# Performance work log

Hardware: AMD Instinct MI355X
Metric: run time of the kernel (lower is better)

The kernel has to match this reference:

```python
import jax, jax.numpy as jnp
import numpy as np
from jax import lax

B = 2; H = 32; W = 32; C = 384
NH = 12; NG = 6; KK = 7; STRIDE = 1; ORF = 2.0
CG = C // NG; HC = C // NH; GH = NH // NG; HID = 4 * C
EPS = 1e-5


def layernorm(x, w, b):
    mu = jnp.mean(x, axis=-1, keepdims=True)
    var = jnp.mean((x - mu) ** 2, axis=-1, keepdims=True)
    return (x - mu) * lax.rsqrt(var + EPS) * w + b


def ref_points(Hk, Wk):
    # normalized reference grid in (-1,1), ordering (y, x) as in _get_ref_points
    ry = ((jnp.arange(Hk, dtype=jnp.float32) + 0.5) / Hk) * 2.0 - 1.0
    rx = ((jnp.arange(Wk, dtype=jnp.float32) + 0.5) / Wk) * 2.0 - 1.0
    return jnp.stack(jnp.meshgrid(ry, rx, indexing='ij'), axis=-1)  # (Hk, Wk, 2)


def grid_sample(img, grid):
    # torch F.grid_sample: bilinear, align_corners=True, padding_mode='zeros'
    # img: (N, Cc, Hi, Wi); grid: (N, ..., 2) with (x, y) in [-1, 1]
    N, Cc, Hi, Wi = img.shape
    out_shape = grid.shape[1:-1]
    g = grid.reshape(N, -1, 2)
    x = (g[..., 0] + 1.0) * 0.5 * (Wi - 1)
    y = (g[..., 1] + 1.0) * 0.5 * (Hi - 1)
    x0 = jnp.floor(x); y0 = jnp.floor(y)
    wx1 = x - x0; wy1 = y - y0
    flat = img.reshape(N, Cc, Hi * Wi)
    M = g.shape[1]
    def gather(ix, iy, wgt):
        valid = (ix >= 0) & (ix <= Wi - 1) & (iy >= 0) & (iy <= Hi - 1)
        idx = (jnp.clip(iy, 0, Hi - 1) * Wi + jnp.clip(ix, 0, Wi - 1)).astype(jnp.int32)
        vals = jnp.take_along_axis(flat, jnp.broadcast_to(idx[:, None, :], (N, Cc, M)), axis=2)
        return vals * (wgt * valid.astype(img.dtype))[:, None, :]
    out = (gather(x0, y0, (1 - wx1) * (1 - wy1))
           + gather(x0 + 1, y0, wx1 * (1 - wy1))
           + gather(x0, y0 + 1, (1 - wx1) * wy1)
           + gather(x0 + 1, y0 + 1, wx1 * wy1))
    return out.reshape((N, Cc) + out_shape)


def setup_inputs() -> dict:
    ks = jax.random.split(jax.random.key(0), 16)
    n = lambda k, s, sc=0.02: jax.random.normal(k, s, jnp.float32) * sc
    return dict(
        x=jax.random.normal(ks[0], (B, H * W, C), jnp.float32),
        norm1_w=jnp.ones((C,), jnp.float32), norm1_b=jnp.zeros((C,), jnp.float32),
        wq=n(ks[1], (C, C)), bq=jnp.zeros((C,), jnp.float32),
        wk=n(ks[2], (C, C)), bk=jnp.zeros((C,), jnp.float32),
        wv=n(ks[3], (C, C)), bv=jnp.zeros((C,), jnp.float32),
        wo=n(ks[4], (C, C)), bo=jnp.zeros((C,), jnp.float32),
        off_dw_w=n(ks[5], (CG, 1, KK, KK)), off_dw_b=jnp.zeros((CG,), jnp.float32),
        off_ln_w=jnp.ones((CG,), jnp.float32), off_ln_b=jnp.zeros((CG,), jnp.float32),
        off_pw_w=n(ks[6], (2, CG)),
        rpe_table=n(ks[7], (NH, 2 * H - 1, 2 * W - 1), 0.01),
        norm2_w=jnp.ones((C,), jnp.float32), norm2_b=jnp.zeros((C,), jnp.float32),
        fc1_w=n(ks[8], (HID, C)), fc1_b=jnp.zeros((HID,), jnp.float32),
        fc2_w=n(ks[9], (C, HID)), fc2_b=jnp.zeros((C,), jnp.float32),
    )


def reference(x, norm1_w, norm1_b, wq, bq, wk, bk, wv, bv, wo, bo,
              off_dw_w, off_dw_b, off_ln_w, off_ln_b, off_pw_w, rpe_table,
              norm2_w, norm2_b, fc1_w, fc1_b, fc2_w, fc2_b):
    Bx, L, Cx = x.shape
    shortcut = x
    xn = layernorm(x, norm1_w, norm1_b)
    xi = xn.reshape(Bx, H, W, Cx).transpose(0, 3, 1, 2)  # (B, C, H, W)

    # proj_q (1x1 conv)
    q = jnp.einsum('bchw,dc->bdhw', xi, wq) + bq[None, :, None, None]

    # offset network on per-group channels
    q_off = q.reshape(Bx * NG, CG, H, W)
    o = lax.conv_general_dilated(q_off, off_dw_w, (STRIDE, STRIDE),
                                 [(KK // 2, KK // 2), (KK // 2, KK // 2)],
                                 dimension_numbers=('NCHW', 'OIHW', 'NCHW'),
                                 feature_group_count=CG) + off_dw_b[None, :, None, None]
    o = layernorm(o.transpose(0, 2, 3, 1), off_ln_w, off_ln_b)  # (Bg, Hk, Wk, CG)
    o = jax.nn.gelu(o, approximate=False)
    offset = jnp.einsum('bhwc,pc->bphw', o, off_pw_w)  # (Bg, 2, Hk, Wk)
    Hk, Wk = offset.shape[2], offset.shape[3]
    ns = Hk * Wk
    orange = jnp.array([1.0 / Hk, 1.0 / Wk], jnp.float32).reshape(1, 2, 1, 1)
    offset = jnp.tanh(offset) * orange * ORF
    offset = offset.transpose(0, 2, 3, 1)  # (Bg, Hk, Wk, 2) (y, x)
    pos = offset + ref_points(Hk, Wk)[None]  # offset_range_factor >= 0 branch

    # deformable sampling of the (normed) feature map
    xs = grid_sample(xi.reshape(Bx * NG, CG, H, W), pos[..., ::-1])  # (Bg, CG, Hk, Wk)
    xs = xs.reshape(Bx, Cx, 1, ns)

    k = (jnp.einsum('bcxn,dc->bdxn', xs, wk) + bk[None, :, None, None]).reshape(Bx * NH, HC, ns)
    v = (jnp.einsum('bcxn,dc->bdxn', xs, wv) + bv[None, :, None, None]).reshape(Bx * NH, HC, ns)
    q_ = q.reshape(Bx * NH, HC, H * W)

    attn = jnp.einsum('bcm,bcn->bmn', q_, k) * (HC ** -0.5)  # (B*NH, HW, ns)

    # continuous relative position bias via grid_sample on rpe_table
    rpe = jnp.broadcast_to(rpe_table[None], (Bx, NH, 2 * H - 1, 2 * W - 1)).reshape(
        Bx * NG, GH, 2 * H - 1, 2 * W - 1)
    qg = ref_points(H, W).reshape(H * W, 2)[None]  # (1, HW, 2)
    disp = (qg[:, :, None, :] - pos.reshape(Bx * NG, ns, 2)[:, None, :, :]) * 0.5  # (Bg, HW, ns, 2)
    bias = grid_sample(rpe, disp[..., ::-1])  # (Bg, GH, HW, ns)
    attn = attn + bias.reshape(Bx * NH, H * W, ns)

    attn = jax.nn.softmax(attn, axis=2)
    out = jnp.einsum('bmn,bcn->bcm', attn, v).reshape(Bx, Cx, H, W)
    y = jnp.einsum('bchw,dc->bdhw', out, wo) + bo[None, :, None, None]
    y = y.transpose(0, 2, 3, 1).reshape(Bx, L, Cx)

    x2 = shortcut + y
    h = layernorm(x2, norm2_w, norm2_b)
    h = jax.nn.gelu(h @ fc1_w.T + fc1_b, approximate=False) @ fc2_w.T + fc2_b
    return x2 + h
```

## Files before the change

### kernel.cpp

```cpp
#include <hip/hip_runtime.h>
#include <math.h>

#define Bc 2
#define Hh 32
#define Ww 32
#define Cc 384
#define NHc 12
#define NGc 6
#define CGc 64
#define HCc 32
#define GHc 2
#define HIDc 1536
#define Lc 1024
#define NSc 1024
#define BGc 12

typedef float f32x4 __attribute__((ext_vector_type(4)));
typedef short bf16x8 __attribute__((ext_vector_type(8)));

__device__ __forceinline__ float gelu_f(float v) {
    return 0.5f * v * (1.f + erff(v * 0.70710678118654752440f));
}

__device__ __forceinline__ unsigned short f2bf(float f) {
    unsigned u = __float_as_uint(f);
    u = (u + 0x7FFF + ((u >> 16) & 1)) >> 16;
    return (unsigned short)u;
}

__device__ __forceinline__ float bf2f(unsigned short u) {
    return __uint_as_float((unsigned)u << 16);
}

__global__ __launch_bounds__(128) void ln_kernel(
    const float* __restrict__ x, const float* __restrict__ w,
    const float* __restrict__ b, unsigned short* __restrict__ out)
{
    __shared__ float l1[2], l2[2];
    int row = blockIdx.x;
    int t = threadIdx.x;
    const float* xr = x + (size_t)row * Cc;
    float v0 = xr[t], v1 = xr[t + 128], v2 = xr[t + 256];
    float s = v0 + v1 + v2;
    #pragma unroll
    for (int o = 32; o; o >>= 1) s += __shfl_down(s, o);
    if ((t & 63) == 0) l1[t >> 6] = s;
    __syncthreads();
    float mu = (l1[0] + l1[1]) * (1.f / Cc);
    float d0 = v0 - mu, d1 = v1 - mu, d2 = v2 - mu;
    float q = d0 * d0 + d1 * d1 + d2 * d2;
    #pragma unroll
    for (int o = 32; o; o >>= 1) q += __shfl_down(q, o);
    if ((t & 63) == 0) l2[t >> 6] = q;
    __syncthreads();
    float rstd = rsqrtf((l2[0] + l2[1]) * (1.f / Cc) + 1e-5f);
    unsigned short* orow = out + (size_t)row * Cc;
    orow[t]       = f2bf(d0 * rstd * w[t]       + b[t]);
    orow[t + 128] = f2bf(d1 * rstd * w[t + 128] + b[t + 128]);
    orow[t + 256] = f2bf(d2 * rstd * w[t + 256] + b[t + 256]);
}

__global__ __launch_bounds__(256) void cast6_kernel(
    const float* __restrict__ wq, const float* __restrict__ wk,
    const float* __restrict__ wv, const float* __restrict__ wo,
    const float* __restrict__ f1, const float* __restrict__ f2,
    unsigned short* __restrict__ dq, unsigned short* __restrict__ dk,
    unsigned short* __restrict__ dv, unsigned short* __restrict__ d_o,
    unsigned short* __restrict__ d1, unsigned short* __restrict__ d2)
{
    int bid = blockIdx.x;
    const float* s; unsigned short* d; int base;
    if (bid < 144)       { s = wq; d = dq;  base = bid; }
    else if (bid < 288)  { s = wk; d = dk;  base = bid - 144; }
    else if (bid < 432)  { s = wv; d = dv;  base = bid - 288; }
    else if (bid < 576)  { s = wo; d = d_o; base = bid - 432; }
    else if (bid < 1152) { s = f1; d = d1;  base = bid - 576; }
    else                 { s = f2; d = d2;  base = bid - 1152; }
    int i = base * 1024 + threadIdx.x * 4;
    float4 v = *(const float4*)(s + i);
    ushort4 u;
    u.x = f2bf(v.x); u.y = f2bf(v.y); u.z = f2bf(v.z); u.w = f2bf(v.w);
    *(ushort4*)(d + i) = u;
}

template<int EPI>
__global__ __launch_bounds__(256) void mfma_gemm(
    const unsigned short* __restrict__ A, const unsigned short* __restrict__ W,
    const float* __restrict__ bias, const float* __restrict__ res,
    void* __restrict__ out1, void* __restrict__ out2, int M, int N, int K)
{
    int w = threadIdx.x >> 6, l = threadIdx.x & 63;
    int col = l & 15, quad = l >> 4;
    int mb = blockIdx.x * 64 + w * 16;
    int n0 = blockIdx.y * 32;
    const unsigned short* Ap = A + (size_t)(mb + col) * K + quad * 8;
    const unsigned short* Wp0 = W + (size_t)(n0 + col) * K + quad * 8;
    const unsigned short* Wp1 = W + (size_t)(n0 + 16 + col) * K + quad * 8;
    f32x4 acc[2] = {};
    #pragma unroll 4
    for (int k0 = 0; k0 < K; k0 += 32) {
        bf16x8 af = *(const bf16x8*)(Ap + k0);
        bf16x8 w0 = *(const bf16x8*)(Wp0 + k0);
        bf16x8 w1 = *(const bf16x8*)(Wp1 + k0);
        acc[0] = __builtin_amdgcn_mfma_f32_16x16x32_bf16(af, w0, acc[0], 0, 0, 0);
        acc[1] = __builtin_amdgcn_mfma_f32_16x16x32_bf16(af, w1, acc[1], 0, 0, 0);
    }
    int bb = mb >> 10, l0 = (mb & 1023) + quad * 4;
    #pragma unroll
    for (int ch = 0; ch < 2; ch++) {
        int n = n0 + ch * 16 + col;
        float bv = bias[n];
        if (EPI == 3) {
            float4 qv;
            qv.x = acc[ch][0] + bv; qv.y = acc[ch][1] + bv;
            qv.z = acc[ch][2] + bv; qv.w = acc[ch][3] + bv;
            *(float4*)&((float*)out1)[((size_t)(bb * Cc + n)) * Lc + l0] = qv;
            unsigned short* q2 = (unsigned short*)out2;
            size_t base = (((size_t)(bb * NHc + (n >> 5))) * Lc + l0) * 32 + (n & 31);
            q2[base]      = f2bf(qv.x);
            q2[base + 32] = f2bf(qv.y);
            q2[base + 64] = f2bf(qv.z);
            q2[base + 96] = f2bf(qv.w);
        } else {
            #pragma unroll
            for (int r = 0; r < 4; r++) {
                size_t m = mb + quad * 4 + r;
                float v = acc[ch][r] + bv;
                if (EPI == 1)
                    ((unsigned short*)out1)[m * N + n] = f2bf(gelu_f(v));
                else
                    ((float*)out1)[m * N + n] = v + res[m * N + n];
            }
        }
    }
}

__global__ __launch_bounds__(256) void mfma_kv(
    const unsigned short* __restrict__ A, const unsigned short* __restrict__ Wk,
    const unsigned short* __restrict__ Wv, const float* __restrict__ bk,
    const float* __restrict__ bv, unsigned short* __restrict__ kout,
    unsigned short* __restrict__ vout, int M, int K)
{
    int w = threadIdx.x >> 6, l = threadIdx.x & 63;
    int col = l & 15, quad = l >> 4;
    int mb = blockIdx.x * 64 + w * 16;
    int n0 = blockIdx.y * 32;
    const unsigned short* Ap = A + (size_t)(mb + col) * K + quad * 8;
    const unsigned short* Wk0 = Wk + (size_t)(n0 + col) * K + quad * 8;
    const unsigned short* Wk1 = Wk + (size_t)(n0 + 16 + col) * K + quad * 8;
    const unsigned short* Wv0 = Wv + (size_t)(n0 + col) * K + quad * 8;
    const unsigned short* Wv1 = Wv + (size_t)(n0 + 16 + col) * K + quad * 8;
    f32x4 ak[2] = {}, av[2] = {};
    #pragma unroll 4
    for (int k0 = 0; k0 < K; k0 += 32) {
        bf16x8 af = *(const bf16x8*)(Ap + k0);
        bf16x8 k0f = *(const bf16x8*)(Wk0 + k0);
        bf16x8 k1f = *(const bf16x8*)(Wk1 + k0);
        bf16x8 v0f = *(const bf16x8*)(Wv0 + k0);
        bf16x8 v1f = *(const bf16x8*)(Wv1 + k0);
        ak[0] = __builtin_amdgcn_mfma_f32_16x16x32_bf16(af, k0f, ak[0], 0, 0, 0);
        ak[1] = __builtin_amdgcn_mfma_f32_16x16x32_bf16(af, k1f, ak[1], 0, 0, 0);
        av[0] = __builtin_amdgcn_mfma_f32_16x16x32_bf16(af, v0f, av[0], 0, 0, 0);
        av[1] = __builtin_amdgcn_mfma_f32_16x16x32_bf16(af, v1f, av[1], 0, 0, 0);
    }
    int bb = mb >> 10, l0 = (mb & 1023) + quad * 4;
    #pragma unroll
    for (int ch = 0; ch < 2; ch++) {
        int n = n0 + ch * 16 + col;
        float bkv = bk[n], bvv = bv[n];
        #pragma unroll
        for (int r = 0; r < 4; r++)
            kout[(size_t)(mb + quad * 4 + r) * Cc + n] = f2bf(ak[ch][r] + bkv);
        ushort4 u;
        u.x = f2bf(av[ch][0] + bvv); u.y = f2bf(av[ch][1] + bvv);
        u.z = f2bf(av[ch][2] + bvv); u.w = f2bf(av[ch][3] + bvv);
        *(ushort4*)&vout[((size_t)(bb * Cc + n)) * NSc + l0] = u;
    }
}

__global__ __launch_bounds__(256) void dwconv_kernel(
    const float* __restrict__ q, const float* __restrict__ wdw,
    const float* __restrict__ bdw, float* __restrict__ o_dw)
{
    int cg = blockIdx.x, bg = blockIdx.y;
    int b = bg / NGc, g = bg % NGc;
    __shared__ float wk_s[49];
    __shared__ float img[1024];
    const float* qp = q + (size_t)(b * Cc + g * CGc + cg) * Lc;
    if (threadIdx.x < 49) wk_s[threadIdx.x] = wdw[cg * 49 + threadIdx.x];
    #pragma unroll
    for (int i = 0; i < 4; i++) img[threadIdx.x + i * 256] = qp[threadIdx.x + i * 256];
    __syncthreads();
    float bias = bdw[cg];
    #pragma unroll
    for (int i = 0; i < 4; i++) {
        int hw = threadIdx.x + i * 256;
        int y = hw >> 5, xx = hw & 31;
        float acc = bias;
        #pragma unroll
        for (int ky = 0; ky < 7; ky++) {
            int yy = y + ky - 3;
            if (yy < 0 || yy > 31) continue;
            #pragma unroll
            for (int kx = 0; kx < 7; kx++) {
                int x2 = xx + kx - 3;
                if (x2 < 0 || x2 > 31) continue;
                acc += img[yy * 32 + x2] * wk_s[ky * 7 + kx];
            }
        }
        o_dw[(size_t)(bg * CGc + cg) * Lc + hw] = acc;
    }
}

__global__ __launch_bounds__(256) void offset_kernel(
    const float* __restrict__ o_dw, const float* __restrict__ lnw,
    const float* __restrict__ lnb, const float* __restrict__ pw,
    float* __restrict__ pos)
{
    int hw = blockIdx.x * 4 + (threadIdx.x >> 6);
    int bg = blockIdx.y;
    int cg = threadIdx.x & 63;
    float v = o_dw[(size_t)(bg * CGc + cg) * Lc + hw];
    float s = v;
    #pragma unroll
    for (int o = 32; o; o >>= 1) s += __shfl_down(s, o);
    s = __shfl(s, 0, 64);
    float mu = s * (1.f / CGc);
    float d = v - mu;
    float q2 = d * d;
    #pragma unroll
    for (int o = 32; o; o >>= 1) q2 += __shfl_down(q2, o);
    q2 = __shfl(q2, 0, 64);
    float rstd = rsqrtf(q2 * (1.f / CGc) + 1e-5f);
    float t = d * rstd * lnw[cg] + lnb[cg];
    float gl = gelu_f(t);
    float sy = gl * pw[cg];
    float sx = gl * pw[CGc + cg];
    #pragma unroll
    for (int o = 32; o; o >>= 1) {
        sy += __shfl_down(sy, o);
        sx += __shfl_down(sx, o);
    }
    if (cg == 0) {
        float offy = tanhf(sy) * 0.0625f;
        float offx = tanhf(sx) * 0.0625f;
        int y = hw >> 5, xx = hw & 31;
        pos[((size_t)bg * Lc + hw) * 2 + 0] = offy + ((y + 0.5f) * (2.f / Hh) - 1.f);
        pos[((size_t)bg * Lc + hw) * 2 + 1] = offx + ((xx + 0.5f) * (2.f / Ww) - 1.f);
    }
}

__global__ __launch_bounds__(256) void sample_kernel(
    const unsigned short* __restrict__ xn, const float* __restrict__ pos,
    unsigned short* __restrict__ xs)
{
    int cg = threadIdx.x & 63;
    int nl = threadIdx.x >> 6;
    int n = blockIdx.x * 4 + nl;
    int bg = blockIdx.y;
    int b = bg / NGc, g = bg % NGc;
    float py = pos[((size_t)bg * NSc + n) * 2 + 0];
    float px = pos[((size_t)bg * NSc + n) * 2 + 1];
    float fx = (px + 1.f) * 0.5f * 31.f;
    float fy = (py + 1.f) * 0.5f * 31.f;
    float x0f = floorf(fx), y0f = floorf(fy);
    int x0 = (int)x0f, y0 = (int)y0f;
    float wx1 = fx - x0f, wy1 = fy - y0f;
    float wx0 = 1.f - wx1, wy0 = 1.f - wy1;
    const unsigned short* base = xn + (size_t)(b * Lc) * Cc + g * CGc + cg;
    float acc = 0.f;
    if (y0 >= 0 && y0 <= 31) {
        if (x0 >= 0 && x0 <= 31) acc += bf2f(base[(size_t)(y0 * 32 + x0) * Cc]) * wx0 * wy0;
        if (x0 + 1 >= 0 && x0 + 1 <= 31) acc += bf2f(base[(size_t)(y0 * 32 + x0 + 1) * Cc]) * wx1 * wy0;
    }
    if (y0 + 1 >= 0 && y0 + 1 <= 31) {
        if (x0 >= 0 && x0 <= 31) acc += bf2f(base[(size_t)((y0 + 1) * 32 + x0) * Cc]) * wx0 * wy1;
        if (x0 + 1 >= 0 && x0 + 1 <= 31) acc += bf2f(base[(size_t)((y0 + 1) * 32 + x0 + 1) * Cc]) * wx1 * wy1;
    }
    xs[((size_t)(b * NSc) + n) * Cc + g * CGc + cg] = f2bf(acc);
}

__global__ __launch_bounds__(256) void attn_kernel(
    const unsigned short* __restrict__ qbf, const unsigned short* __restrict__ kbf,
    const unsigned short* __restrict__ vtb, const float* __restrict__ pos,
    const float* __restrict__ rpe, unsigned short* __restrict__ attno)
{
    __shared__ float o_smem[2112];
    __shared__ unsigned short p_bf[4][16 * 72];
    __shared__ float ml_s[4][2][16];
    unsigned short* rpe_s = (unsigned short*)o_smem;

    int m0 = blockIdx.x * 16;
    int h = blockIdx.y, b = blockIdx.z;
    int tid = threadIdx.x;
    int w = tid >> 6, l = tid & 63;
    int col = l & 15, quad = l >> 4;

    const float* tb = rpe + (size_t)h * 3969;
    for (int i = tid; i < 63 * 65; i += 256) {
        int row = i / 65, cx = i - row * 65;
        rpe_s[i] = (cx < 63) ? f2bf(tb[row * 63 + cx] * 1.44269504f) : 0;
    }

    bf16x8 qfrag = *(const bf16x8*)(qbf +
        ((((size_t)(b * NHc + h)) * Lc + m0 + col) * 32 + quad * 8));

    float qgy = ((m0 >> 5) + 0.5f) * (2.f / 32.f) - 1.f;
    float qgx0 = (((m0 & 31) + quad * 4) + 0.5f) * (2.f / 32.f) - 1.f;

    const unsigned short* kb_ = kbf + (size_t)b * NSc * Cc + h * HCc;
    const unsigned short* vb_ = vtb + ((size_t)(b * Cc + h * HCc)) * NSc;
    const float2* pp = (const float2*)(pos + (size_t)(b * NGc + (h >> 1)) * NSc * 2);

    float run_m[4] = {-3.0e38f, -3.0e38f, -3.0e38f, -3.0e38f};
    float run_l[4] = {0.f, 0.f, 0.f, 0.f};
    f32x4 O0 = {0.f, 0.f, 0.f, 0.f};
    f32x4 O1 = {0.f, 0.f, 0.f, 0.f};

    __syncthreads();

    for (int it = 0; it < 4; it++) {
        int n0 = w * 256 + it * 64;
        f32x4 s[4];
        #pragma unroll
        for (int ch = 0; ch < 4; ch++) {
            bf16x8 kf = *(const bf16x8*)(kb_ +
                ((size_t)(n0 + ch * 16 + col) * Cc + quad * 8));
            f32x4 z = {0.f, 0.f, 0.f, 0.f};
            s[ch] = __builtin_amdgcn_mfma_f32_16x16x32_bf16(qfrag, kf, z, 0, 0, 0);
        }
        #pragma unroll
        for (int ch = 0; ch < 4; ch++) {
            int n = n0 + ch * 16 + col;
            float2 pyx = pp[n];
            float fy = ((qgy - pyx.x) * 0.5f + 1.f) * 31.f;
            float y0f = floorf(fy);
            int iy = (int)y0f;
            float wy1 = fy - y0f, wy0 = 1.f - wy1;
            bool y0ok = (unsigned)iy <= 62u;
            bool y1ok = (unsigned)(iy + 1) <= 62u;
            const unsigned short* r0 = rpe_s + iy * 65;
            float fx0 = ((qgx0 - pyx.y) * 0.5f + 1.f) * 31.f;
            #pragma unroll
            for (int r = 0; r < 4; r++) {
                float fx = fx0 + r * 0.96875f;
                float x0f = floorf(fx);
                int ix = (int)x0f;
                float wx1 = fx - x0f, wx0 = 1.f - wx1;
                bool x0ok = (unsigned)ix <= 62u;
                bool x1ok = (unsigned)(ix + 1) <= 62u;
                float bias = 0.f;
                if (y0ok) {
                    if (x0ok) bias += bf2f(r0[ix]) * wy0 * wx0;
                    if (x1ok) bias += bf2f(r0[ix + 1]) * wy0 * wx1;
                }
                if (y1ok) {
                    if (x0ok) bias += bf2f(r0[65 + ix]) * wy1 * wx0;
                    if (x1ok) bias += bf2f(r0[65 + ix + 1]) * wy1 * wx1;
                }
                s[ch][r] = s[ch][r] * 0.25506974f + bias;
            }
        }
        float nm[4], alpha[4];
        #pragma unroll
        for (int r = 0; r < 4; r++) {
            float mx = fmaxf(fmaxf(s[0][r], s[1][r]), fmaxf(s[2][r], s[3][r]));
            #pragma unroll
            for (int msk = 1; msk < 16; msk <<= 1)
                mx = fmaxf(mx, __shfl_xor(mx, msk));
            nm[r] = fmaxf(run_m[r], mx);
            alpha[r] = exp2f(run_m[r] - nm[r]);
            run_m[r] = nm[r];
        }
        float rowsum[4] = {0.f, 0.f, 0.f, 0.f};
        #pragma unroll
        for (int ch = 0; ch < 4; ch++)
            #pragma unroll
            for (int r = 0; r < 4; r++) {
                float e = exp2f(s[ch][r] - nm[r]);
                s[ch][r] = e;
                rowsum[r] += e;
            }
        #pragma unroll
        for (int r = 0; r < 4; r++) {
            float sm = rowsum[r];
            #pragma unroll
            for (int msk = 1; msk < 16; msk <<= 1)
                sm += __shfl_xor(sm, msk);
            run_l[r] = run_l[r] * alpha[r] + sm;
        }
        #pragma unroll
        for (int ch = 0; ch < 4; ch++)
            #pragma unroll
            for (int r = 0; r < 4; r++)
                p_bf[w][(quad * 4 + r) * 72 + ch * 16 + col] = f2bf(s[ch][r]);
        #pragma unroll
        for (int r = 0; r < 4; r++) { O0[r] *= alpha[r]; O1[r] *= alpha[r]; }
        #pragma unroll
        for (int half = 0; half < 2; half++) {
            bf16x8 pf = *(const bf16x8*)&p_bf[w][col * 72 + half * 32 + quad * 8];
            bf16x8 v0 = *(const bf16x8*)(vb_ +
                ((size_t)col * NSc + n0 + half * 32 + quad * 8));
            O0 = __builtin_amdgcn_mfma_f32_16x16x32_bf16(pf, v0, O0, 0, 0, 0);
            bf16x8 v1 = *(const bf16x8*)(vb_ +
                ((size_t)(col + 16) * NSc + n0 + half * 32 + quad * 8));
            O1 = __builtin_amdgcn_mfma_f32_16x16x32_bf16(pf, v1, O1, 0, 0, 0);
        }
    }
    __syncthreads();
    float* o_s = o_smem;
    #pragma unroll
    for (int r = 0; r < 4; r++) {
        int m = quad * 4 + r;
        o_s[w * 528 + m * 33 + col] = O0[r];
        o_s[w * 528 + m * 33 + col + 16] = O1[r];
    }
    if (col == 0) {
        #pragma unroll
        for (int r = 0; r < 4; r++) {
            ml_s[w][0][quad * 4 + r] = run_m[r];
            ml_s[w][1][quad * 4 + r] = run_l[r];
        }
    }
    __syncthreads();
    for (int i = tid; i < 512; i += 256) {
        int m = i >> 5, c = i & 31;
        float fm = fmaxf(fmaxf(ml_s[0][0][m], ml_s[1][0][m]),
                         fmaxf(ml_s[2][0][m], ml_s[3][0][m]));
        float lsum = 0.f, osum = 0.f;
        #pragma unroll
        for (int ww = 0; ww < 4; ww++) {
            float sc = exp2f(ml_s[ww][0][m] - fm);
            lsum += ml_s[ww][1][m] * sc;
            osum += o_s[ww * 528 + m * 33 + c] * sc;
        }
        attno[((size_t)(b * Lc) + m0 + m) * Cc + h * HCc + c] = f2bf(osum / lsum);
    }
}

extern "C" void kernel_launch(void* const* d_in, const int* in_sizes, int n_in,
                              void* d_out, int out_size, void* d_ws, size_t ws_size,
                              hipStream_t stream)
{
    const float* x    = (const float*)d_in[0];
    const float* n1w  = (const float*)d_in[1];
    const float* n1b  = (const float*)d_in[2];
    const float* wq   = (const float*)d_in[3];
    const float* bq   = (const float*)d_in[4];
    const float* wk   = (const float*)d_in[5];
    const float* bk   = (const float*)d_in[6];
    const float* wv   = (const float*)d_in[7];
    const float* bv   = (const float*)d_in[8];
    const float* wo   = (const float*)d_in[9];
    const float* bo   = (const float*)d_in[10];
    const float* dw_w = (const float*)d_in[11];
    const float* dw_b = (const float*)d_in[12];
    const float* lnw  = (const float*)d_in[13];
    const float* lnb  = (const float*)d_in[14];
    const float* pw_w = (const float*)d_in[15];
    const float* rpe  = (const float*)d_in[16];
    const float* n2w  = (const float*)d_in[17];
    const float* n2b  = (const float*)d_in[18];
    const float* fc1w = (const float*)d_in[19];
    const float* fc1b = (const float*)d_in[20];
    const float* fc2w = (const float*)d_in[21];
    const float* fc2b = (const float*)d_in[22];
    float* out = (float*)d_out;

    float* ws = (float*)d_ws;
    unsigned short* xnbf = (unsigned short*)ws;
    float*          qb   = ws + 393216;
    unsigned short* qbf  = (unsigned short*)(ws + 1179648);
    unsigned short* h1bf = (unsigned short*)ws;
    float* odw   = ws + 1572864;
    unsigned short* xln2bf = (unsigned short*)(ws + 1572864);
    float* posb  = ws + 2359296;
    unsigned short* xsbf = (unsigned short*)(ws + 2383872);
    unsigned short* kbf  = (unsigned short*)(ws + 2777088);
    unsigned short* vtb  = (unsigned short*)(ws + 3170304);
    unsigned short* attnbf = (unsigned short*)(ws + 3563520);
    float* x2    = ws + 3956736;
    unsigned short* wqbf   = (unsigned short*)(ws + 4743168);
    unsigned short* wkbf   = (unsigned short*)(ws + 4816896);
    unsigned short* wvbf   = (unsigned short*)(ws + 4890624);
    unsigned short* wobf   = (unsigned short*)(ws + 4964352);
    unsigned short* fc1wbf = (unsigned short*)(ws + 5038080);
    unsigned short* fc2wbf = (unsigned short*)(ws + 5332992);

    cast6_kernel<<<1728, 256, 0, stream>>>(
        wq, wk, wv, wo, fc1w, fc2w, wqbf, wkbf, wvbf, wobf, fc1wbf, fc2wbf);
    ln_kernel<<<Bc * Lc, 128, 0, stream>>>(x, n1w, n1b, xnbf);
    mfma_gemm<3><<<dim3(Bc * Lc / 64, Cc / 32), 256, 0, stream>>>(
        xnbf, wqbf, bq, x, qb, qbf, Bc * Lc, Cc, Cc);
    dwconv_kernel<<<dim3(CGc, BGc), 256, 0, stream>>>(qb, dw_w, dw_b, odw);
    offset_kernel<<<dim3(Lc / 4, BGc), 256, 0, stream>>>(odw, lnw, lnb, pw_w, posb);
    sample_kernel<<<dim3(NSc / 4, BGc), 256, 0, stream>>>(xnbf, posb, xsbf);
    mfma_kv<<<dim3(Bc * NSc / 64, Cc / 32), 256, 0, stream>>>(
        xsbf, wkbf, wvbf, bk, bv, kbf, vtb, Bc * NSc, Cc);
    attn_kernel<<<dim3(Lc / 16, NHc, Bc), 256, 0, stream>>>(
        qbf, kbf, vtb, posb, rpe, attnbf);
    mfma_gemm<2><<<dim3(Bc * Lc / 64, Cc / 32), 256, 0, stream>>>(
        attnbf, wobf, bo, x, x2, x2, Bc * Lc, Cc, Cc);
    ln_kernel<<<Bc * Lc, 128, 0, stream>>>(x2, n2w, n2b, xln2bf);
    mfma_gemm<1><<<dim3(Bc * Lc / 64, HIDc / 32), 256, 0, stream>>>(
        xln2bf, fc1wbf, fc1b, x2, h1bf, h1bf, Bc * Lc, HIDc, Cc);
    mfma_gemm<2><<<dim3(Bc * Lc / 64, Cc / 32), 256, 0, stream>>>(
        h1bf, fc2wbf, fc2b, x2, out, out, Bc * Lc, Cc, HIDc);
}
```

Measured before the change: 298.1 us.

## Prefetch K/V fragments in attention, pad RPE table, store Q as bf16

The attention loop now preloads the next K fragments and the current V fragments into registers ahead of the MFMAs so global-load latency overlaps with compute. The RPE shared table gets a one-element zero border, which removes the per-sample bounds checks in the bilinear bias lookup. The Q projection's channel-major copy for the depthwise conv is now written as bf16 instead of fp32, halving that traffic. Costs are more registers, a slightly larger shared buffer, and lower precision on the conv input feeding the offset path.

```diff
diff --git a/kernel.cpp b/kernel.cpp
--- a/kernel.cpp
+++ b/kernel.cpp
@@ -111,16 +111,15 @@
         int n = n0 + ch * 16 + col;
         float bv = bias[n];
         if (EPI == 3) {
-            float4 qv;
-            qv.x = acc[ch][0] + bv; qv.y = acc[ch][1] + bv;
-            qv.z = acc[ch][2] + bv; qv.w = acc[ch][3] + bv;
-            *(float4*)&((float*)out1)[((size_t)(bb * Cc + n)) * Lc + l0] = qv;
+            unsigned short u0 = f2bf(acc[ch][0] + bv);
+            unsigned short u1 = f2bf(acc[ch][1] + bv);
+            unsigned short u2 = f2bf(acc[ch][2] + bv);
+            unsigned short u3 = f2bf(acc[ch][3] + bv);
+            ushort4 qv = {u0, u1, u2, u3};
+            *(ushort4*)&((unsigned short*)out1)[((size_t)(bb * Cc + n)) * Lc + l0] = qv;
             unsigned short* q2 = (unsigned short*)out2;
             size_t base = (((size_t)(bb * NHc + (n >> 5))) * Lc + l0) * 32 + (n & 31);
-            q2[base]      = f2bf(qv.x);
-            q2[base + 32] = f2bf(qv.y);
-            q2[base + 64] = f2bf(qv.z);
-            q2[base + 96] = f2bf(qv.w);
+            q2[base] = u0; q2[base + 32] = u1; q2[base + 64] = u2; q2[base + 96] = u3;
         } else {
             #pragma unroll
             for (int r = 0; r < 4; r++) {
@@ -179,17 +178,18 @@
 }
 
 __global__ __launch_bounds__(256) void dwconv_kernel(
-    const float* __restrict__ q, const float* __restrict__ wdw,
+    const unsigned short* __restrict__ q, const float* __restrict__ wdw,
     const float* __restrict__ bdw, float* __restrict__ o_dw)
 {
     int cg = blockIdx.x, bg = blockIdx.y;
     int b = bg / NGc, g = bg % NGc;
     __shared__ float wk_s[49];
     __shared__ float img[1024];
-    const float* qp = q + (size_t)(b * Cc + g * CGc + cg) * Lc;
+    const unsigned short* qp = q + (size_t)(b * Cc + g * CGc + cg) * Lc;
     if (threadIdx.x < 49) wk_s[threadIdx.x] = wdw[cg * 49 + threadIdx.x];
     #pragma unroll
-    for (int i = 0; i < 4; i++) img[threadIdx.x + i * 256] = qp[threadIdx.x + i * 256];
+    for (int i = 0; i < 4; i++)
+        img[threadIdx.x + i * 256] = bf2f(qp[threadIdx.x + i * 256]);
     __syncthreads();
     float bias = bdw[cg];
     #pragma unroll
@@ -285,7 +285,7 @@
     const unsigned short* __restrict__ vtb, const float* __restrict__ pos,
     const float* __restrict__ rpe, unsigned short* __restrict__ attno)
 {
-    __shared__ float o_smem[2112];
+    __shared__ float o_smem[2145];
     __shared__ unsigned short p_bf[4][16 * 72];
     __shared__ float ml_s[4][2][16];
     unsigned short* rpe_s = (unsigned short*)o_smem;
@@ -297,9 +297,12 @@
     int col = l & 15, quad = l >> 4;
 
     const float* tb = rpe + (size_t)h * 3969;
-    for (int i = tid; i < 63 * 65; i += 256) {
-        int row = i / 65, cx = i - row * 65;
-        rpe_s[i] = (cx < 63) ? f2bf(tb[row * 63 + cx] * 1.44269504f) : 0;
+    for (int i = tid; i < 65 * 66; i += 256) {
+        int row = i / 66, cx = i - row * 66;
+        unsigned short v = 0;
+        if (row >= 1 && row <= 63 && cx >= 1 && cx <= 63)
+            v = f2bf(tb[(row - 1) * 63 + (cx - 1)] * 1.44269504f);
+        rpe_s[i] = v;
     }
 
     bf16x8 qfrag = *(const bf16x8*)(qbf +
@@ -317,17 +320,41 @@
     f32x4 O0 = {0.f, 0.f, 0.f, 0.f};
     f32x4 O1 = {0.f, 0.f, 0.f, 0.f};
 
+    bf16x8 kcur[4];
+    {
+        int n0 = w * 256;
+        #pragma unroll
+        for (int ch = 0; ch < 4; ch++)
+            kcur[ch] = *(const bf16x8*)(kb_ +
+                ((size_t)(n0 + ch * 16 + col) * Cc + quad * 8));
+    }
+
     __syncthreads();
 
+    #pragma unroll
     for (int it = 0; it < 4; it++) {
         int n0 = w * 256 + it * 64;
+        bf16x8 vf[4];
+        #pragma unroll
+        for (int half = 0; half < 2; half++) {
+            vf[half * 2]     = *(const bf16x8*)(vb_ +
+                ((size_t)col * NSc + n0 + half * 32 + quad * 8));
+            vf[half * 2 + 1] = *(const bf16x8*)(vb_ +
+                ((size_t)(col + 16) * NSc + n0 + half * 32 + quad * 8));
+        }
+        bf16x8 knext[4];
+        if (it < 3) {
+            int n1 = n0 + 64;
+            #pragma unroll
+            for (int ch = 0; ch < 4; ch++)
+                knext[ch] = *(const bf16x8*)(kb_ +
+                    ((size_t)(n1 + ch * 16 + col) * Cc + quad * 8));
+        }
         f32x4 s[4];
         #pragma unroll
         for (int ch = 0; ch < 4; ch++) {
-            bf16x8 kf = *(const bf16x8*)(kb_ +
-                ((size_t)(n0 + ch * 16 + col) * Cc + quad * 8));
             f32x4 z = {0.f, 0.f, 0.f, 0.f};
-            s[ch] = __builtin_amdgcn_mfma_f32_16x16x32_bf16(qfrag, kf, z, 0, 0, 0);
+            s[ch] = __builtin_amdgcn_mfma_f32_16x16x32_bf16(qfrag, kcur[ch], z, 0, 0, 0);
         }
         #pragma unroll
         for (int ch = 0; ch < 4; ch++) {
@@ -335,30 +362,18 @@
             float2 pyx = pp[n];
             float fy = ((qgy - pyx.x) * 0.5f + 1.f) * 31.f;
             float y0f = floorf(fy);
-            int iy = (int)y0f;
             float wy1 = fy - y0f, wy0 = 1.f - wy1;
-            bool y0ok = (unsigned)iy <= 62u;
-            bool y1ok = (unsigned)(iy + 1) <= 62u;
-            const unsigned short* r0 = rpe_s + iy * 65;
-            float fx0 = ((qgx0 - pyx.y) * 0.5f + 1.f) * 31.f;
+            const unsigned short* r0 = rpe_s + ((int)y0f + 1) * 66;
+            float fx0 = ((qgx0 - pyx.y) * 0.5f + 1.f) * 31.f + 1.f;
             #pragma unroll
             for (int r = 0; r < 4; r++) {
                 float fx = fx0 + r * 0.96875f;
                 float x0f = floorf(fx);
                 int ix = (int)x0f;
                 float wx1 = fx - x0f, wx0 = 1.f - wx1;
-                bool x0ok = (unsigned)ix <= 62u;
-                bool x1ok = (unsigned)(ix + 1) <= 62u;
-                float bias = 0.f;
-                if (y0ok) {
-                    if (x0ok) bias += bf2f(r0[ix]) * wy0 * wx0;
-                    if (x1ok) bias += bf2f(r0[ix + 1]) * wy0 * wx1;
-                }
-                if (y1ok) {
-                    if (x0ok) bias += bf2f(r0[65 + ix]) * wy1 * wx0;
-                    if (x1ok) bias += bf2f(r0[65 + ix + 1]) * wy1 * wx1;
-                }
-                s[ch][r] = s[ch][r] * 0.25506974f + bias;
+                float b0 = bf2f(r0[ix]) * wx0 + bf2f(r0[ix + 1]) * wx1;
+                float b1 = bf2f(r0[66 + ix]) * wx0 + bf2f(r0[66 + ix + 1]) * wx1;
+                s[ch][r] = s[ch][r] * 0.25506974f + (b0 * wy0 + b1 * wy1);
             }
         }
         float nm[4], alpha[4];
@@ -399,13 +414,11 @@
         #pragma unroll
         for (int half = 0; half < 2; half++) {
             bf16x8 pf = *(const bf16x8*)&p_bf[w][col * 72 + half * 32 + quad * 8];
-            bf16x8 v0 = *(const bf16x8*)(vb_ +
-                ((size_t)col * NSc + n0 + half * 32 + quad * 8));
-            O0 = __builtin_amdgcn_mfma_f32_16x16x32_bf16(pf, v0, O0, 0, 0, 0);
-            bf16x8 v1 = *(const bf16x8*)(vb_ +
-                ((size_t)(col + 16) * NSc + n0 + half * 32 + quad * 8));
-            O1 = __builtin_amdgcn_mfma_f32_16x16x32_bf16(pf, v1, O1, 0, 0, 0);
-        }
+            O0 = __builtin_amdgcn_mfma_f32_16x16x32_bf16(pf, vf[half * 2], O0, 0, 0, 0);
+            O1 = __builtin_amdgcn_mfma_f32_16x16x32_bf16(pf, vf[half * 2 + 1], O1, 0, 0, 0);
+        }
+        #pragma unroll
+        for (int ch = 0; ch < 4; ch++) kcur[ch] = knext[ch];
     }
     __syncthreads();
     float* o_s = o_smem;
@@ -469,7 +482,7 @@
 
     float* ws = (float*)d_ws;
     unsigned short* xnbf = (unsigned short*)ws;
-    float*          qb   = ws + 393216;
+    unsigned short* qb16 = (unsigned short*)(ws + 393216);
     unsigned short* qbf  = (unsigned short*)(ws + 1179648);
     unsigned short* h1bf = (unsigned short*)ws;
     float* odw   = ws + 1572864;
@@ -491,8 +504,8 @@
         wq, wk, wv, wo, fc1w, fc2w, wqbf, wkbf, wvbf, wobf, fc1wbf, fc2wbf);
     ln_kernel<<<Bc * Lc, 128, 0, stream>>>(x, n1w, n1b, xnbf);
     mfma_gemm<3><<<dim3(Bc * Lc / 64, Cc / 32), 256, 0, stream>>>(
-        xnbf, wqbf, bq, x, qb, qbf, Bc * Lc, Cc, Cc);
-    dwconv_kernel<<<dim3(CGc, BGc), 256, 0, stream>>>(qb, dw_w, dw_b, odw);
+        xnbf, wqbf, bq, x, qb16, qbf, Bc * Lc, Cc, Cc);
+    dwconv_kernel<<<dim3(CGc, BGc), 256, 0, stream>>>(qb16, dw_w, dw_b, odw);
     offset_kernel<<<dim3(Lc / 4, BGc), 256, 0, stream>>>(odw, lnw, lnb, pw_w, posb);
     sample_kernel<<<dim3(NSc / 4, BGc), 256, 0, stream>>>(xnbf, posb, xsbf);
     mfma_kv<<<dim3(Bc * NSc / 64, Cc / 32), 256, 0, stream>>>(
```

New measurement: 345.1 us. +15.7%, slower.
